# Kernel tuning notes

Hardware: AMD Instinct MI355X
Metric: run time of the kernel (lower is better)

The kernel has to match this reference:

```python
import jax, jax.numpy as jnp
import numpy as np

IN_SIZE = 4096
BATCH = 8192


def setup_inputs() -> dict:
    key = jax.random.key(0)
    kx, kw, kb = jax.random.split(key, 3)
    x = jax.random.normal(kx, (BATCH, IN_SIZE), dtype=jnp.float32)
    # init_parameters: uniform_(-1e-4, 1e-4)
    weight = jax.random.uniform(kw, (IN_SIZE,), dtype=jnp.float32, minval=-1e-4, maxval=1e-4)
    bias = jax.random.uniform(kb, (IN_SIZE,), dtype=jnp.float32, minval=-1e-4, maxval=1e-4)
    return {"x": x, "weight": weight, "bias": bias}


def reference(x, weight, bias):
    # x @ diagflat(weight) + bias  ==  x * weight + bias (broadcast over batch)
    return x * weight + bias
```

## Files before the change

kernel.cpp:

```cpp
#include <hip/hip_runtime.h>
#include <hip/hip_bf16.h>


#define IN_SIZE   4096
#define COLS4     (IN_SIZE / 4)

__global__ __launch_bounds__(256) void diag_linear_kernel(
    const float4* __restrict__ x,
    const float4* __restrict__ w,
    const float4* __restrict__ b,
    float4* __restrict__ out,
    int n4)
{
    int idx = blockIdx.x * blockDim.x + threadIdx.x;
    if (idx >= n4) return;

    int c4 = idx & (COLS4 - 1);

    float4 xv = x[idx];
    float4 wv = w[c4];
    float4 bv = b[c4];

    float4 o;
    o.x = fmaf(xv.x, wv.x, bv.x);
    o.y = fmaf(xv.y, wv.y, bv.y);
    o.z = fmaf(xv.z, wv.z, bv.z);
    o.w = fmaf(xv.w, wv.w, bv.w);

    out[idx] = o;
}

extern "C" void kernel_launch(void* const* d_in, const int* in_sizes, int n_in,
                              void* d_out, int out_size, void* d_ws, size_t ws_size,
                              hipStream_t stream) {
    const float4* x = (const float4*)d_in[0];
    const float4* w = (const float4*)d_in[1];
    const float4* b = (const float4*)d_in[2];
    float4* out = (float4*)d_out;

    int n4 = out_size / 4;
    int block = 256;
    int grid = (n4 + block - 1) / block;

    diag_linear_kernel<<<grid, block, 0, stream>>>(x, w, b, out, n4);
}
```

Baseline: 226.0 us.

## Use grid-stride rows with hoisted weight/bias and nontemporal stores

Replaces the one-thread-per-float4 launch with a fixed grid of 2048 blocks that stride over rows. Each thread loads its weight and bias column once and reuses them across rows, and it writes output with nontemporal stores so the streamed result does not pollute the cache. This is meant to cut per-thread overhead and redundant w/b loads in a purely bandwidth-bound kernel. It hardcodes BATCH and removes the bounds check, so it only works for this exact shape.

```diff
diff --git a/kernel.cpp b/kernel.cpp
--- a/kernel.cpp
+++ b/kernel.cpp
@@ -2,45 +2,41 @@
 #include <hip/hip_bf16.h>
 
 
+typedef float f32x4 __attribute__((ext_vector_type(4)));
+
 #define IN_SIZE   4096
 #define COLS4     (IN_SIZE / 4)
+#define BATCH     8192
 
 __global__ __launch_bounds__(256) void diag_linear_kernel(
-    const float4* __restrict__ x,
-    const float4* __restrict__ w,
-    const float4* __restrict__ b,
-    float4* __restrict__ out,
-    int n4)
+    const f32x4* __restrict__ x,
+    const f32x4* __restrict__ w,
+    const f32x4* __restrict__ b,
+    f32x4* __restrict__ out)
 {
-    int idx = blockIdx.x * blockDim.x + threadIdx.x;
-    if (idx >= n4) return;
+    const int tid        = blockIdx.x * blockDim.x + threadIdx.x;
+    const int c4         = tid & (COLS4 - 1);
+    const int row0       = tid >> 10;
+    const int row_stride = (gridDim.x * blockDim.x) >> 10;
 
-    int c4 = idx & (COLS4 - 1);
+    const f32x4 wv = w[c4];
+    const f32x4 bv = b[c4];
 
-    float4 xv = x[idx];
-    float4 wv = w[c4];
-    float4 bv = b[c4];
-
-    float4 o;
-    o.x = fmaf(xv.x, wv.x, bv.x);
-    o.y = fmaf(xv.y, wv.y, bv.y);
-    o.z = fmaf(xv.z, wv.z, bv.z);
-    o.w = fmaf(xv.w, wv.w, bv.w);
-
-    out[idx] = o;
+    for (int r = row0; r < BATCH; r += row_stride) {
+        const int idx = r * COLS4 + c4;
+        f32x4 xv = x[idx];
+        f32x4 o = xv * wv + bv;
+        __builtin_nontemporal_store(o, &out[idx]);
+    }
 }
 
 extern "C" void kernel_launch(void* const* d_in, const int* in_sizes, int n_in,
                               void* d_out, int out_size, void* d_ws, size_t ws_size,
                               hipStream_t stream) {
-    const float4* x = (const float4*)d_in[0];
-    const float4* w = (const float4*)d_in[1];
-    const float4* b = (const float4*)d_in[2];
-    float4* out = (float4*)d_out;
+    const f32x4* x = (const f32x4*)d_in[0];
+    const f32x4* w = (const f32x4*)d_in[1];
+    const f32x4* b = (const f32x4*)d_in[2];
+    f32x4* out = (f32x4*)d_out;
 
-    int n4 = out_size / 4;
-    int block = 256;
-    int grid = (n4 + block - 1) / block;
-
-    diag_linear_kernel<<<grid, block, 0, stream>>>(x, w, b, out, n4);
+    diag_linear_kernel<<<2048, 256, 0, stream>>>(x, w, b, out);
 }
```

New measurement: 234.5 us. 1.04x slower.
